# Kernel tuning notes

Measured on AMD Instinct MI355X. Metric: run time of the kernel, lower is better.

## Reference

```python
import jax, jax.numpy as jnp
import numpy as np
from jax.lax import associative_scan

D_H = 1024

def _binary_operator(e_i, e_j):
    a_i, kv_i = e_i
    a_j, kv_j = e_j
    return (a_j * a_i, a_j * kv_i + kv_j)

def setup_inputs() -> dict:
    key = jax.random.key(0)
    k1, k2 = jax.random.split(key)
    x = jax.random.normal(k1, (4, 4096, 3 * D_H), dtype=jnp.float32)
    carry = jax.random.normal(k2, (4, D_H), dtype=jnp.float32)
    return {"x": x, "carry": carry}

def reference(x, carry):
    d_h = D_H
    inp = jnp.tanh(x[:, :, :d_h])                      # (B, S, d_h)
    gates = jax.nn.sigmoid(x[:, :, d_h:])              # (B, S, 2*d_h)
    input_gate, output_gate = jnp.split(gates, 2, axis=-1)
    forget_gate = 1.0 - input_gate                     # tied gates
    scan_ins = inp * input_gate                        # (B, S, d_h)
    # inject carry at t=0: h_0 = f_0*carry + i_0*in_0
    scan_ins = scan_ins.at[:, 0, :].set(scan_ins[:, 0, :] + carry * forget_gate[:, 0, :])
    _, h = associative_scan(_binary_operator, (forget_gate, scan_ins), axis=1)
    y = jnp.tanh(h) * output_gate                      # (B, S, d_h)
    h_last = h[:, -1, :]
    return (h_last, y)
```

## Files before the change

### kernel.cpp

```cpp
#include <hip/hip_runtime.h>


#define B_SZ 4
#define T_LEN 4096
#define DH 1024
#define ROW4 (3 * DH / 4)
#define CHUNKS 512
#define CLEN (T_LEN / CHUNKS)
#define SUBC 8
#define SUPERS (CHUNKS / SUBC)

typedef float vf4 __attribute__((ext_vector_type(4)));

__device__ __forceinline__ float fsig(float v) {
    return __builtin_amdgcn_rcpf(1.0f + __expf(-v));
}
__device__ __forceinline__ float ftanh(float v) {
    return 1.0f - 2.0f * __builtin_amdgcn_rcpf(__expf(2.0f * v) + 1.0f);
}

__device__ __forceinline__ void step_ab(float xi, float xg, float& A, float& Bv) {
    const float ig = fsig(xg);
    const float a = 1.f - ig;
    A *= a;
    Bv = a * Bv + ftanh(xi) * ig;
}

__global__ __launch_bounds__(256) void glru_pass1(const float* __restrict__ x,
                                                  float4* __restrict__ Aag,
                                                  float4* __restrict__ Bag) {
    const int c = blockIdx.x;
    const int b = blockIdx.y;
    const int d4 = threadIdx.x;
    const float4* base = (const float4*)x + (size_t)(b * T_LEN + c * CLEN) * ROW4;

    float4 vi[CLEN], vg[CLEN];
    #pragma unroll
    for (int t = 0; t < CLEN; ++t) {
        vi[t] = base[(size_t)t * ROW4 + d4];
        vg[t] = base[(size_t)t * ROW4 + 256 + d4];
    }

    float4 A = make_float4(1.f, 1.f, 1.f, 1.f);
    float4 Bv = make_float4(0.f, 0.f, 0.f, 0.f);
    #pragma unroll
    for (int t = 0; t < CLEN; ++t) {
        step_ab(vi[t].x, vg[t].x, A.x, Bv.x);
        step_ab(vi[t].y, vg[t].y, A.y, Bv.y);
        step_ab(vi[t].z, vg[t].z, A.z, Bv.z);
        step_ab(vi[t].w, vg[t].w, A.w, Bv.w);
    }
    const int o = (b * CHUNKS + c) * 256 + d4;
    Aag[o] = A;
    Bag[o] = Bv;
}

__global__ __launch_bounds__(256) void glru_p2a(const float* __restrict__ Aag,
                                                const float* __restrict__ Bag,
                                                float* __restrict__ Asup,
                                                float* __restrict__ Bsup) {
    const int tid = blockIdx.x * 256 + threadIdx.x;
    const int d = tid & (DH - 1);
    const int su = (tid >> 10) & (SUPERS - 1);
    const int b = tid >> 16;

    float As = 1.f, Bs = 0.f;
    #pragma unroll
    for (int j = 0; j < SUBC; ++j) {
        const size_t o = ((size_t)(b * CHUNKS + su * SUBC + j) << 10) + d;
        const float a = Aag[o];
        As *= a;
        Bs = a * Bs + Bag[o];
    }
    const int so = (b * SUPERS + su) * DH + d;
    Asup[so] = As;
    Bsup[so] = Bs;
}

__global__ __launch_bounds__(256) void glru_p2b(const float* __restrict__ Asup,
                                                const float* __restrict__ Bsup,
                                                const float* __restrict__ carry,
                                                float* __restrict__ hsup,
                                                float* __restrict__ hlast) {
    const int idx = blockIdx.x * 256 + threadIdx.x;
    const int b = idx >> 10;
    const int d = idx & (DH - 1);
    float h = carry[idx];
    #pragma unroll 8
    for (int s = 0; s < SUPERS; ++s) {
        const int o = (b * SUPERS + s) * DH + d;
        hsup[o] = h;
        h = Asup[o] * h + Bsup[o];
    }
    hlast[idx] = h;
}

__global__ __launch_bounds__(256) void glru_p2c(const float* __restrict__ Aag,
                                                const float* __restrict__ Bag,
                                                const float* __restrict__ hsup,
                                                float* __restrict__ hinit) {
    const int tid = blockIdx.x * 256 + threadIdx.x;
    const int d = tid & (DH - 1);
    const int su = (tid >> 10) & (SUPERS - 1);
    const int b = tid >> 16;

    float h = hsup[(b * SUPERS + su) * DH + d];
    #pragma unroll
    for (int j = 0; j < SUBC; ++j) {
        const size_t o = ((size_t)(b * CHUNKS + su * SUBC + j) << 10) + d;
        hinit[o] = h;
        h = Aag[o] * h + Bag[o];
    }
}

__global__ __launch_bounds__(256) void glru_pass3(const float* __restrict__ x,
                                                  const float4* __restrict__ hinit,
                                                  float4* __restrict__ y) {
    const int c = blockIdx.x;
    const int b = blockIdx.y;
    const int d4 = threadIdx.x;
    const float4* base = (const float4*)x + (size_t)(b * T_LEN + c * CLEN) * ROW4;
    float4* yb = y + (size_t)(b * T_LEN + c * CLEN) * 256;

    float4 vi[CLEN], vg[CLEN];
    #pragma unroll
    for (int t = 0; t < CLEN; ++t) {
        vi[t] = base[(size_t)t * ROW4 + d4];
        vg[t] = base[(size_t)t * ROW4 + 256 + d4];
    }
    float4 h = hinit[(b * CHUNKS + c) * 256 + d4];

    #pragma unroll
    for (int t = 0; t < CLEN; ++t) {
        const float4 vo = base[(size_t)t * ROW4 + 512 + d4];
        float4 out;
        {
            float ig = fsig(vg[t].x); float a = 1.f - ig;
            h.x = a * h.x + ftanh(vi[t].x) * ig;
            out.x = ftanh(h.x) * fsig(vo.x);
        }
        {
            float ig = fsig(vg[t].y); float a = 1.f - ig;
            h.y = a * h.y + ftanh(vi[t].y) * ig;
            out.y = ftanh(h.y) * fsig(vo.y);
        }
        {
            float ig = fsig(vg[t].z); float a = 1.f - ig;
            h.z = a * h.z + ftanh(vi[t].z) * ig;
            out.z = ftanh(h.z) * fsig(vo.z);
        }
        {
            float ig = fsig(vg[t].w); float a = 1.f - ig;
            h.w = a * h.w + ftanh(vi[t].w) * ig;
            out.w = ftanh(h.w) * fsig(vo.w);
        }
        vf4 outv;
        outv.x = out.x; outv.y = out.y; outv.z = out.z; outv.w = out.w;
        __builtin_nontemporal_store(outv, (vf4*)&yb[(size_t)t * 256 + d4]);
    }
}

extern "C" void kernel_launch(void* const* d_in, const int* in_sizes, int n_in,
                              void* d_out, int out_size, void* d_ws, size_t ws_size,
                              hipStream_t stream) {
    const float* x = (const float*)d_in[0];
    const float* carry = (const float*)d_in[1];

    float* hlast = (float*)d_out;
    float4* y = (float4*)((float*)d_out + B_SZ * DH);

    float* Aag = (float*)d_ws;
    float* Bag = Aag + (size_t)B_SZ * CHUNKS * DH;
    float* hinit = Bag + (size_t)B_SZ * CHUNKS * DH;
    float* Asup = hinit + (size_t)B_SZ * CHUNKS * DH;
    float* Bsup = Asup + (size_t)B_SZ * SUPERS * DH;
    float* hsup = Bsup + (size_t)B_SZ * SUPERS * DH;

    glru_pass1<<<dim3(CHUNKS, B_SZ), 256, 0, stream>>>(x, (float4*)Aag, (float4*)Bag);
    glru_p2a<<<(B_SZ * SUPERS * DH) / 256, 256, 0, stream>>>(Aag, Bag, Asup, Bsup);
    glru_p2b<<<16, 256, 0, stream>>>(Asup, Bsup, carry, hsup, hlast);
    glru_p2c<<<(B_SZ * SUPERS * DH) / 256, 256, 0, stream>>>(Aag, Bag, hsup, hinit);
    glru_pass3<<<dim3(CHUNKS, B_SZ), 256, 0, stream>>>(x, (const float4*)hinit, y);
}
```

Before: 318.0 us.

## Fuse scan passes into one cooperative kernel with grid syncs

Replaces the five separate kernel launches with one cooperative kernel of 1024 blocks that uses grid-wide syncs between the chunk-aggregate, super-chunk combine, sequential carry scan and output phases. Chunk count drops to 256 per batch with chunk length 16 and sub-chunk groups of 16. The p2c pass is removed: each output block recomputes its starting state from the super-chunk state and the preceding chunk aggregates. Loads are now done in groups of 4 timesteps to reduce register pressure. It removes launch overhead and one intermediate buffer, but requires all 1024 blocks to be co-resident at four blocks per CU and adds grid-sync cost. If the cooperative launch fails it falls back to four ordinary launches.

```diff
diff --git a/kernel.cpp b/kernel.cpp
--- a/kernel.cpp
+++ b/kernel.cpp
@@ -1,14 +1,16 @@
 #include <hip/hip_runtime.h>
+#include <hip/hip_cooperative_groups.h>
 
 
 #define B_SZ 4
 #define T_LEN 4096
 #define DH 1024
 #define ROW4 (3 * DH / 4)
-#define CHUNKS 512
-#define CLEN (T_LEN / CHUNKS)
-#define SUBC 8
-#define SUPERS (CHUNKS / SUBC)
+#define CPB 256
+#define CLEN (T_LEN / CPB)
+#define SUBC 16
+#define SUPERS (CPB / SUBC)
+#define GRID (B_SZ * CPB)
 
 typedef float vf4 __attribute__((ext_vector_type(4)));
 
@@ -18,7 +20,6 @@
 __device__ __forceinline__ float ftanh(float v) {
     return 1.0f - 2.0f * __builtin_amdgcn_rcpf(__expf(2.0f * v) + 1.0f);
 }
-
 __device__ __forceinline__ void step_ab(float xi, float xg, float& A, float& Bv) {
     const float ig = fsig(xg);
     const float a = 1.f - ig;
@@ -26,67 +27,66 @@
     Bv = a * Bv + ftanh(xi) * ig;
 }
 
-__global__ __launch_bounds__(256) void glru_pass1(const float* __restrict__ x,
-                                                  float4* __restrict__ Aag,
-                                                  float4* __restrict__ Bag) {
-    const int c = blockIdx.x;
-    const int b = blockIdx.y;
-    const int d4 = threadIdx.x;
+
+__device__ __forceinline__ void phase1(int blk, int d4, const float* __restrict__ x,
+                                       float4* __restrict__ Aag, float4* __restrict__ Bag) {
+    const int b = blk >> 8;
+    const int c = blk & (CPB - 1);
     const float4* base = (const float4*)x + (size_t)(b * T_LEN + c * CLEN) * ROW4;
-
-    float4 vi[CLEN], vg[CLEN];
-    #pragma unroll
-    for (int t = 0; t < CLEN; ++t) {
-        vi[t] = base[(size_t)t * ROW4 + d4];
-        vg[t] = base[(size_t)t * ROW4 + 256 + d4];
-    }
 
     float4 A = make_float4(1.f, 1.f, 1.f, 1.f);
     float4 Bv = make_float4(0.f, 0.f, 0.f, 0.f);
     #pragma unroll
-    for (int t = 0; t < CLEN; ++t) {
-        step_ab(vi[t].x, vg[t].x, A.x, Bv.x);
-        step_ab(vi[t].y, vg[t].y, A.y, Bv.y);
-        step_ab(vi[t].z, vg[t].z, A.z, Bv.z);
-        step_ab(vi[t].w, vg[t].w, A.w, Bv.w);
-    }
-    const int o = (b * CHUNKS + c) * 256 + d4;
+    for (int g = 0; g < CLEN / 4; ++g) {
+        float4 vi[4], vg[4];
+        #pragma unroll
+        for (int t = 0; t < 4; ++t) {
+            const size_t r = (size_t)(g * 4 + t) * ROW4;
+            vi[t] = base[r + d4];
+            vg[t] = base[r + 256 + d4];
+        }
+        #pragma unroll
+        for (int t = 0; t < 4; ++t) {
+            step_ab(vi[t].x, vg[t].x, A.x, Bv.x);
+            step_ab(vi[t].y, vg[t].y, A.y, Bv.y);
+            step_ab(vi[t].z, vg[t].z, A.z, Bv.z);
+            step_ab(vi[t].w, vg[t].w, A.w, Bv.w);
+        }
+    }
+    const int o = blk * 256 + d4;
     Aag[o] = A;
     Bag[o] = Bv;
 }
 
-__global__ __launch_bounds__(256) void glru_p2a(const float* __restrict__ Aag,
-                                                const float* __restrict__ Bag,
-                                                float* __restrict__ Asup,
-                                                float* __restrict__ Bsup) {
-    const int tid = blockIdx.x * 256 + threadIdx.x;
+__device__ __forceinline__ void phase2a(int blk, int tx, const float* __restrict__ Aagf,
+                                        const float* __restrict__ Bagf,
+                                        float* __restrict__ Asup, float* __restrict__ Bsup) {
+    const int tid = blk * 256 + tx;
     const int d = tid & (DH - 1);
     const int su = (tid >> 10) & (SUPERS - 1);
-    const int b = tid >> 16;
-
+    const int b = tid >> 14;
     float As = 1.f, Bs = 0.f;
     #pragma unroll
     for (int j = 0; j < SUBC; ++j) {
-        const size_t o = ((size_t)(b * CHUNKS + su * SUBC + j) << 10) + d;
-        const float a = Aag[o];
+        const size_t o = ((size_t)(b * CPB + su * SUBC + j) << 10) + d;
+        const float a = Aagf[o];
         As *= a;
-        Bs = a * Bs + Bag[o];
+        Bs = a * Bs + Bagf[o];
     }
     const int so = (b * SUPERS + su) * DH + d;
     Asup[so] = As;
     Bsup[so] = Bs;
 }
 
-__global__ __launch_bounds__(256) void glru_p2b(const float* __restrict__ Asup,
-                                                const float* __restrict__ Bsup,
-                                                const float* __restrict__ carry,
-                                                float* __restrict__ hsup,
-                                                float* __restrict__ hlast) {
-    const int idx = blockIdx.x * 256 + threadIdx.x;
+__device__ __forceinline__ void phase2b(int blk, int tx, const float* __restrict__ Asup,
+                                        const float* __restrict__ Bsup,
+                                        const float* __restrict__ carry,
+                                        float* __restrict__ hsup, float* __restrict__ hlast) {
+    const int idx = blk * 256 + tx;
     const int b = idx >> 10;
     const int d = idx & (DH - 1);
     float h = carry[idx];
-    #pragma unroll 8
+    #pragma unroll
     for (int s = 0; s < SUPERS; ++s) {
         const int o = (b * SUPERS + s) * DH + d;
         hsup[o] = h;
@@ -95,69 +95,115 @@
     hlast[idx] = h;
 }
 
-__global__ __launch_bounds__(256) void glru_p2c(const float* __restrict__ Aag,
-                                                const float* __restrict__ Bag,
-                                                const float* __restrict__ hsup,
-                                                float* __restrict__ hinit) {
-    const int tid = blockIdx.x * 256 + threadIdx.x;
-    const int d = tid & (DH - 1);
-    const int su = (tid >> 10) & (SUPERS - 1);
-    const int b = tid >> 16;
-
-    float h = hsup[(b * SUPERS + su) * DH + d];
-    #pragma unroll
-    for (int j = 0; j < SUBC; ++j) {
-        const size_t o = ((size_t)(b * CHUNKS + su * SUBC + j) << 10) + d;
-        hinit[o] = h;
-        h = Aag[o] * h + Bag[o];
-    }
-}
-
-__global__ __launch_bounds__(256) void glru_pass3(const float* __restrict__ x,
-                                                  const float4* __restrict__ hinit,
-                                                  float4* __restrict__ y) {
-    const int c = blockIdx.x;
-    const int b = blockIdx.y;
-    const int d4 = threadIdx.x;
+__device__ __forceinline__ void phase3(int blk, int d4, const float* __restrict__ x,
+                                       const float4* __restrict__ Aag,
+                                       const float4* __restrict__ Bag,
+                                       const float* __restrict__ hsup,
+                                       float4* __restrict__ y) {
+    const int b = blk >> 8;
+    const int c = blk & (CPB - 1);
+    const int su = c / SUBC;
+
+    float4 h = ((const float4*)hsup)[(b * SUPERS + su) * 256 + d4];
+    for (int j = su * SUBC; j < c; ++j) {
+        const int o = (b * CPB + j) * 256 + d4;
+        const float4 a4 = Aag[o];
+        const float4 b4 = Bag[o];
+        h.x = fmaf(a4.x, h.x, b4.x);
+        h.y = fmaf(a4.y, h.y, b4.y);
+        h.z = fmaf(a4.z, h.z, b4.z);
+        h.w = fmaf(a4.w, h.w, b4.w);
+    }
+
     const float4* base = (const float4*)x + (size_t)(b * T_LEN + c * CLEN) * ROW4;
     float4* yb = y + (size_t)(b * T_LEN + c * CLEN) * 256;
-
-    float4 vi[CLEN], vg[CLEN];
-    #pragma unroll
-    for (int t = 0; t < CLEN; ++t) {
-        vi[t] = base[(size_t)t * ROW4 + d4];
-        vg[t] = base[(size_t)t * ROW4 + 256 + d4];
-    }
-    float4 h = hinit[(b * CHUNKS + c) * 256 + d4];
-
-    #pragma unroll
-    for (int t = 0; t < CLEN; ++t) {
-        const float4 vo = base[(size_t)t * ROW4 + 512 + d4];
-        float4 out;
-        {
-            float ig = fsig(vg[t].x); float a = 1.f - ig;
-            h.x = a * h.x + ftanh(vi[t].x) * ig;
-            out.x = ftanh(h.x) * fsig(vo.x);
-        }
-        {
-            float ig = fsig(vg[t].y); float a = 1.f - ig;
-            h.y = a * h.y + ftanh(vi[t].y) * ig;
-            out.y = ftanh(h.y) * fsig(vo.y);
-        }
-        {
-            float ig = fsig(vg[t].z); float a = 1.f - ig;
-            h.z = a * h.z + ftanh(vi[t].z) * ig;
-            out.z = ftanh(h.z) * fsig(vo.z);
-        }
-        {
-            float ig = fsig(vg[t].w); float a = 1.f - ig;
-            h.w = a * h.w + ftanh(vi[t].w) * ig;
-            out.w = ftanh(h.w) * fsig(vo.w);
-        }
-        vf4 outv;
-        outv.x = out.x; outv.y = out.y; outv.z = out.z; outv.w = out.w;
-        __builtin_nontemporal_store(outv, (vf4*)&yb[(size_t)t * 256 + d4]);
-    }
+    #pragma unroll
+    for (int g = 0; g < CLEN / 4; ++g) {
+        float4 vi[4], vg[4], vo[4];
+        #pragma unroll
+        for (int t = 0; t < 4; ++t) {
+            const size_t r = (size_t)(g * 4 + t) * ROW4;
+            vi[t] = base[r + d4];
+            vg[t] = base[r + 256 + d4];
+            vo[t] = base[r + 512 + d4];
+        }
+        #pragma unroll
+        for (int t = 0; t < 4; ++t) {
+            float4 out;
+            {
+                float ig = fsig(vg[t].x); float a = 1.f - ig;
+                h.x = a * h.x + ftanh(vi[t].x) * ig;
+                out.x = ftanh(h.x) * fsig(vo[t].x);
+            }
+            {
+                float ig = fsig(vg[t].y); float a = 1.f - ig;
+                h.y = a * h.y + ftanh(vi[t].y) * ig;
+                out.y = ftanh(h.y) * fsig(vo[t].y);
+            }
+            {
+                float ig = fsig(vg[t].z); float a = 1.f - ig;
+                h.z = a * h.z + ftanh(vi[t].z) * ig;
+                out.z = ftanh(h.z) * fsig(vo[t].z);
+            }
+            {
+                float ig = fsig(vg[t].w); float a = 1.f - ig;
+                h.w = a * h.w + ftanh(vi[t].w) * ig;
+                out.w = ftanh(h.w) * fsig(vo[t].w);
+            }
+            vf4 ov;
+            ov.x = out.x; ov.y = out.y; ov.z = out.z; ov.w = out.w;
+            __builtin_nontemporal_store(ov, (vf4*)&yb[(size_t)(g * 4 + t) * 256 + d4]);
+        }
+    }
+}
+
+__global__ __launch_bounds__(256, 4) void glru_fused(const float* __restrict__ x,
+                                                     const float* __restrict__ carry,
+                                                     float4* __restrict__ Aag,
+                                                     float4* __restrict__ Bag,
+                                                     float* __restrict__ Asup,
+                                                     float* __restrict__ Bsup,
+                                                     float* __restrict__ hsup,
+                                                     float* __restrict__ hlast,
+                                                     float4* __restrict__ y) {
+    const int blk = blockIdx.x;
+    const int tx = threadIdx.x;
+
+    phase1(blk, tx, x, Aag, Bag);
+    cooperative_groups::this_grid().sync();
+
+    if (blk < (B_SZ * SUPERS * DH) / 256)
+        phase2a(blk, tx, (const float*)Aag, (const float*)Bag, Asup, Bsup);
+    cooperative_groups::this_grid().sync();
+
+    if (blk < (B_SZ * DH) / 256)
+        phase2b(blk, tx, Asup, Bsup, carry, hsup, hlast);
+    cooperative_groups::this_grid().sync();
+
+    phase3(blk, tx, x, Aag, Bag, hsup, y);
+}
+
+__global__ __launch_bounds__(256) void k_p1(const float* __restrict__ x,
+                                            float4* __restrict__ Aag, float4* __restrict__ Bag) {
+    phase1(blockIdx.x, threadIdx.x, x, Aag, Bag);
+}
+__global__ __launch_bounds__(256) void k_p2a(const float* __restrict__ Aagf,
+                                             const float* __restrict__ Bagf,
+                                             float* __restrict__ Asup, float* __restrict__ Bsup) {
+    phase2a(blockIdx.x, threadIdx.x, Aagf, Bagf, Asup, Bsup);
+}
+__global__ __launch_bounds__(256) void k_p2b(const float* __restrict__ Asup,
+                                             const float* __restrict__ Bsup,
+                                             const float* __restrict__ carry,
+                                             float* __restrict__ hsup, float* __restrict__ hlast) {
+    phase2b(blockIdx.x, threadIdx.x, Asup, Bsup, carry, hsup, hlast);
+}
+__global__ __launch_bounds__(256) void k_p3(const float* __restrict__ x,
+                                            const float4* __restrict__ Aag,
+                                            const float4* __restrict__ Bag,
+                                            const float* __restrict__ hsup,
+                                            float4* __restrict__ y) {
+    phase3(blockIdx.x, threadIdx.x, x, Aag, Bag, hsup, y);
 }
 
 extern "C" void kernel_launch(void* const* d_in, const int* in_sizes, int n_in,
@@ -169,16 +215,21 @@
     float* hlast = (float*)d_out;
     float4* y = (float4*)((float*)d_out + B_SZ * DH);
 
-    float* Aag = (float*)d_ws;
-    float* Bag = Aag + (size_t)B_SZ * CHUNKS * DH;
-    float* hinit = Bag + (size_t)B_SZ * CHUNKS * DH;
-    float* Asup = hinit + (size_t)B_SZ * CHUNKS * DH;
-    float* Bsup = Asup + (size_t)B_SZ * SUPERS * DH;
-    float* hsup = Bsup + (size_t)B_SZ * SUPERS * DH;
-
-    glru_pass1<<<dim3(CHUNKS, B_SZ), 256, 0, stream>>>(x, (float4*)Aag, (float4*)Bag);
-    glru_p2a<<<(B_SZ * SUPERS * DH) / 256, 256, 0, stream>>>(Aag, Bag, Asup, Bsup);
-    glru_p2b<<<16, 256, 0, stream>>>(Asup, Bsup, carry, hsup, hlast);
-    glru_p2c<<<(B_SZ * SUPERS * DH) / 256, 256, 0, stream>>>(Aag, Bag, hsup, hinit);
-    glru_pass3<<<dim3(CHUNKS, B_SZ), 256, 0, stream>>>(x, (const float4*)hinit, y);
-}
+    float4* Aag = (float4*)d_ws;
+    float4* Bag = Aag + (size_t)GRID * 256;
+    float* Asup = (float*)(Bag + (size_t)GRID * 256);
+    float* Bsup = Asup + B_SZ * SUPERS * DH;
+    float* hsup = Bsup + B_SZ * SUPERS * DH;
+
+    void* args[] = {(void*)&x, (void*)&carry, (void*)&Aag, (void*)&Bag,
+                    (void*)&Asup, (void*)&Bsup, (void*)&hsup, (void*)&hlast, (void*)&y};
+    hipError_t err = hipLaunchCooperativeKernel(reinterpret_cast<const void*>(&glru_fused),
+                                                dim3(GRID), dim3(256), args, 0u, stream);
+    if (err != hipSuccess) {
+        k_p1<<<GRID, 256, 0, stream>>>(x, Aag, Bag);
+        k_p2a<<<(B_SZ * SUPERS * DH) / 256, 256, 0, stream>>>((const float*)Aag,
+                                                              (const float*)Bag, Asup, Bsup);
+        k_p2b<<<(B_SZ * DH) / 256, 256, 0, stream>>>(Asup, Bsup, carry, hsup, hlast);
+        k_p3<<<GRID, 256, 0, stream>>>(x, Aag, Bag, hsup, y);
+    }
+}
```

Result: slower. 628.7 us (+97.7%).

## Fuse per-chunk carry propagation into output pass and shrink super-chunk size

Applied to the files above, without the earlier changes.

Drops the separate p2c kernel that wrote per-chunk initial states. The output pass now starts from the super-chunk state and replays up to SUBC-1 chunk aggregates itself. SUBC goes from 8 to 4 so that replay stays short, which doubles the number of super-chunks the serial p2b loop must walk. The output pass also loads x in groups of 4 timesteps instead of preloading all 8, to reduce register pressure. Together these remove one launch and the hinit write/read round trip.

```diff
diff --git a/kernel.cpp b/kernel.cpp
--- a/kernel.cpp
+++ b/kernel.cpp
@@ -5,10 +5,10 @@
 #define T_LEN 4096
 #define DH 1024
 #define ROW4 (3 * DH / 4)
-#define CHUNKS 512
-#define CLEN (T_LEN / CHUNKS)
-#define SUBC 8
-#define SUPERS (CHUNKS / SUBC)
+#define CPB 512
+#define CLEN (T_LEN / CPB)
+#define SUBC 4
+#define SUPERS (CPB / SUBC)
 
 typedef float vf4 __attribute__((ext_vector_type(4)));
 
@@ -18,7 +18,6 @@
 __device__ __forceinline__ float ftanh(float v) {
     return 1.0f - 2.0f * __builtin_amdgcn_rcpf(__expf(2.0f * v) + 1.0f);
 }
-
 __device__ __forceinline__ void step_ab(float xi, float xg, float& A, float& Bv) {
     const float ig = fsig(xg);
     const float a = 1.f - ig;
@@ -26,9 +25,9 @@
     Bv = a * Bv + ftanh(xi) * ig;
 }
 
-__global__ __launch_bounds__(256) void glru_pass1(const float* __restrict__ x,
-                                                  float4* __restrict__ Aag,
-                                                  float4* __restrict__ Bag) {
+__global__ __launch_bounds__(256) void glru_p1(const float* __restrict__ x,
+                                               float4* __restrict__ Aag,
+                                               float4* __restrict__ Bag) {
     const int c = blockIdx.x;
     const int b = blockIdx.y;
     const int d4 = threadIdx.x;
@@ -40,7 +39,6 @@
         vi[t] = base[(size_t)t * ROW4 + d4];
         vg[t] = base[(size_t)t * ROW4 + 256 + d4];
     }
-
     float4 A = make_float4(1.f, 1.f, 1.f, 1.f);
     float4 Bv = make_float4(0.f, 0.f, 0.f, 0.f);
     #pragma unroll
@@ -50,27 +48,27 @@
         step_ab(vi[t].z, vg[t].z, A.z, Bv.z);
         step_ab(vi[t].w, vg[t].w, A.w, Bv.w);
     }
-    const int o = (b * CHUNKS + c) * 256 + d4;
+    const int o = (b * CPB + c) * 256 + d4;
     Aag[o] = A;
     Bag[o] = Bv;
 }
 
-__global__ __launch_bounds__(256) void glru_p2a(const float* __restrict__ Aag,
-                                                const float* __restrict__ Bag,
+__global__ __launch_bounds__(256) void glru_p2a(const float* __restrict__ Aagf,
+                                                const float* __restrict__ Bagf,
                                                 float* __restrict__ Asup,
                                                 float* __restrict__ Bsup) {
     const int tid = blockIdx.x * 256 + threadIdx.x;
     const int d = tid & (DH - 1);
     const int su = (tid >> 10) & (SUPERS - 1);
-    const int b = tid >> 16;
+    const int b = tid >> 17;
 
     float As = 1.f, Bs = 0.f;
     #pragma unroll
     for (int j = 0; j < SUBC; ++j) {
-        const size_t o = ((size_t)(b * CHUNKS + su * SUBC + j) << 10) + d;
-        const float a = Aag[o];
+        const size_t o = ((size_t)(b * CPB + su * SUBC + j) << 10) + d;
+        const float a = Aagf[o];
         As *= a;
-        Bs = a * Bs + Bag[o];
+        Bs = a * Bs + Bagf[o];
     }
     const int so = (b * SUPERS + su) * DH + d;
     Asup[so] = As;
@@ -95,68 +93,67 @@
     hlast[idx] = h;
 }
 
-__global__ __launch_bounds__(256) void glru_p2c(const float* __restrict__ Aag,
-                                                const float* __restrict__ Bag,
-                                                const float* __restrict__ hsup,
-                                                float* __restrict__ hinit) {
-    const int tid = blockIdx.x * 256 + threadIdx.x;
-    const int d = tid & (DH - 1);
-    const int su = (tid >> 10) & (SUPERS - 1);
-    const int b = tid >> 16;
-
-    float h = hsup[(b * SUPERS + su) * DH + d];
-    #pragma unroll
-    for (int j = 0; j < SUBC; ++j) {
-        const size_t o = ((size_t)(b * CHUNKS + su * SUBC + j) << 10) + d;
-        hinit[o] = h;
-        h = Aag[o] * h + Bag[o];
-    }
-}
-
-__global__ __launch_bounds__(256) void glru_pass3(const float* __restrict__ x,
-                                                  const float4* __restrict__ hinit,
-                                                  float4* __restrict__ y) {
+__global__ __launch_bounds__(256) void glru_p3(const float* __restrict__ x,
+                                               const float4* __restrict__ Aag,
+                                               const float4* __restrict__ Bag,
+                                               const float* __restrict__ hsup,
+                                               float4* __restrict__ y) {
     const int c = blockIdx.x;
     const int b = blockIdx.y;
     const int d4 = threadIdx.x;
+    const int su = c / SUBC;
+
+    float4 h = ((const float4*)hsup)[(b * SUPERS + su) * 256 + d4];
+    for (int j = su * SUBC; j < c; ++j) {
+        const int o = (b * CPB + j) * 256 + d4;
+        const float4 a4 = Aag[o];
+        const float4 b4 = Bag[o];
+        h.x = fmaf(a4.x, h.x, b4.x);
+        h.y = fmaf(a4.y, h.y, b4.y);
+        h.z = fmaf(a4.z, h.z, b4.z);
+        h.w = fmaf(a4.w, h.w, b4.w);
+    }
+
     const float4* base = (const float4*)x + (size_t)(b * T_LEN + c * CLEN) * ROW4;
     float4* yb = y + (size_t)(b * T_LEN + c * CLEN) * 256;
 
-    float4 vi[CLEN], vg[CLEN];
     #pragma unroll
-    for (int t = 0; t < CLEN; ++t) {
-        vi[t] = base[(size_t)t * ROW4 + d4];
-        vg[t] = base[(size_t)t * ROW4 + 256 + d4];
-    }
-    float4 h = hinit[(b * CHUNKS + c) * 256 + d4];
-
-    #pragma unroll
-    for (int t = 0; t < CLEN; ++t) {
-        const float4 vo = base[(size_t)t * ROW4 + 512 + d4];
-        float4 out;
-        {
-            float ig = fsig(vg[t].x); float a = 1.f - ig;
-            h.x = a * h.x + ftanh(vi[t].x) * ig;
-            out.x = ftanh(h.x) * fsig(vo.x);
+    for (int g = 0; g < CLEN / 4; ++g) {
+        float4 vi[4], vg[4], vo[4];
+        #pragma unroll
+        for (int t = 0; t < 4; ++t) {
+            const size_t r = (size_t)(g * 4 + t) * ROW4;
+            vi[t] = base[r + d4];
+            vg[t] = base[r + 256 + d4];
+            vo[t] = base[r + 512 + d4];
         }
-        {
-            float ig = fsig(vg[t].y); float a = 1.f - ig;
-            h.y = a * h.y + ftanh(vi[t].y) * ig;
-            out.y = ftanh(h.y) * fsig(vo.y);
+        #pragma unroll
+        for (int t = 0; t < 4; ++t) {
+            float4 out;
+            {
+                float ig = fsig(vg[t].x); float a = 1.f - ig;
+                h.x = a * h.x + ftanh(vi[t].x) * ig;
+                out.x = ftanh(h.x) * fsig(vo[t].x);
+            }
+            {
+                float ig = fsig(vg[t].y); float a = 1.f - ig;
+                h.y = a * h.y + ftanh(vi[t].y) * ig;
+                out.y = ftanh(h.y) * fsig(vo[t].y);
+            }
+            {
+                float ig = fsig(vg[t].z); float a = 1.f - ig;
+                h.z = a * h.z + ftanh(vi[t].z) * ig;
+                out.z = ftanh(h.z) * fsig(vo[t].z);
+            }
+            {
+                float ig = fsig(vg[t].w); float a = 1.f - ig;
+                h.w = a * h.w + ftanh(vi[t].w) * ig;
+                out.w = ftanh(h.w) * fsig(vo[t].w);
+            }
+            vf4 ov;
+            ov.x = out.x; ov.y = out.y; ov.z = out.z; ov.w = out.w;
+            __builtin_nontemporal_store(ov, (vf4*)&yb[(size_t)(g * 4 + t) * 256 + d4]);
         }
-        {
-            float ig = fsig(vg[t].z); float a = 1.f - ig;
-            h.z = a * h.z + ftanh(vi[t].z) * ig;
-            out.z = ftanh(h.z) * fsig(vo.z);
-        }
-        {
-            float ig = fsig(vg[t].w); float a = 1.f - ig;
-            h.w = a * h.w + ftanh(vi[t].w) * ig;
-            out.w = ftanh(h.w) * fsig(vo.w);
-        }
-        vf4 outv;
-        outv.x = out.x; outv.y = out.y; outv.z = out.z; outv.w = out.w;
-        __builtin_nontemporal_store(outv, (vf4*)&yb[(size_t)t * 256 + d4]);
     }
 }
 
@@ -169,16 +166,15 @@
     float* hlast = (float*)d_out;
     float4* y = (float4*)((float*)d_out + B_SZ * DH);
 
-    float* Aag = (float*)d_ws;
-    float* Bag = Aag + (size_t)B_SZ * CHUNKS * DH;
-    float* hinit = Bag + (size_t)B_SZ * CHUNKS * DH;
-    float* Asup = hinit + (size_t)B_SZ * CHUNKS * DH;
-    float* Bsup = Asup + (size_t)B_SZ * SUPERS * DH;
-    float* hsup = Bsup + (size_t)B_SZ * SUPERS * DH;
+    float4* Aag = (float4*)d_ws;
+    float4* Bag = Aag + (size_t)B_SZ * CPB * 256;
+    float* Asup = (float*)(Bag + (size_t)B_SZ * CPB * 256);
+    float* Bsup = Asup + B_SZ * SUPERS * DH;
+    float* hsup = Bsup + B_SZ * SUPERS * DH;
 
-    glru_pass1<<<dim3(CHUNKS, B_SZ), 256, 0, stream>>>(x, (float4*)Aag, (float4*)Bag);
-    glru_p2a<<<(B_SZ * SUPERS * DH) / 256, 256, 0, stream>>>(Aag, Bag, Asup, Bsup);
-    glru_p2b<<<16, 256, 0, stream>>>(Asup, Bsup, carry, hsup, hlast);
-    glru_p2c<<<(B_SZ * SUPERS * DH) / 256, 256, 0, stream>>>(Aag, Bag, hsup, hinit);
-    glru_pass3<<<dim3(CHUNKS, B_SZ), 256, 0, stream>>>(x, (const float4*)hinit, y);
+    glru_p1<<<dim3(CPB, B_SZ), 256, 0, stream>>>(x, Aag, Bag);
+    glru_p2a<<<(B_SZ * SUPERS * DH) / 256, 256, 0, stream>>>((const float*)Aag,
+                                                             (const float*)Bag, Asup, Bsup);
+    glru_p2b<<<(B_SZ * DH) / 256, 256, 0, stream>>>(Asup, Bsup, carry, hsup, hlast);
+    glru_p3<<<dim3(CPB, B_SZ), 256, 0, stream>>>(x, Aag, Bag, hsup, y);
 }
```

Measured after the change: 325.6 us. 1.02x slower.
